# Performance work log

Measured on AMD Instinct MI355X. Metric: run time of the kernel, lower is better.

Reference implementation:

```python
import jax, jax.numpy as jnp
import numpy as np


def _dsepconv(inp, vert, horiz, offx, offy, mask):
    # inp: [B,C,H,W]; vert/horiz: [B,F,H,W]; offx/offy/mask: [B,F*F,H,W]
    B, C, H, W = inp.shape
    F = vert.shape[1]
    FF = F * F
    dt = inp.dtype
    k = jnp.arange(FF)
    ki = (k // F).astype(dt)   # vertical tap index i
    kj = (k % F).astype(dt)    # horizontal tap index j
    half = jnp.asarray((F - 1) / 2.0, dt)
    ys = jnp.arange(H, dtype=dt)
    xs = jnp.arange(W, dtype=dt)
    # per-pixel deformable sample positions, [B,FF,H,W]
    py = offy + ys[None, None, :, None] + (ki - half)[None, :, None, None]
    px = offx + xs[None, None, None, :] + (kj - half)[None, :, None, None]
    py = jnp.clip(py, 0.0, H - 1)
    px = jnp.clip(px, 0.0, W - 1)
    y0f = jnp.floor(py)
    x0f = jnp.floor(px)
    wy = py - y0f   # bilinear fractional weights
    wx = px - x0f
    y0 = y0f.astype(jnp.int32)
    x0 = x0f.astype(jnp.int32)
    y1 = jnp.minimum(y0 + 1, H - 1)
    x1 = jnp.minimum(x0 + 1, W - 1)

    inp_flat = inp.reshape(B, C, H * W)

    def gather(yi, xi):
        # flat spatial gather per batch element -> [B,C,FF,H,W]
        idx = (yi * W + xi).reshape(B, FF * H * W)
        g = jax.vmap(lambda im, ix: im[:, ix])(inp_flat, idx)
        return g.reshape(B, C, FF, H, W)

    g00 = gather(y0, x0)
    g01 = gather(y0, x1)
    g10 = gather(y1, x0)
    g11 = gather(y1, x1)
    wy_ = wy[:, None]  # [B,1,FF,H,W]
    wx_ = wx[:, None]
    samp = (g00 * (1 - wy_) * (1 - wx_)
            + g01 * (1 - wy_) * wx_
            + g10 * wy_ * (1 - wx_)
            + g11 * wy_ * wx_)  # [B,C,FF,H,W]
    # separable mask-weighted tap weights: vert[i]*horiz[j]*mask[k]
    wtap = vert[:, k // F] * horiz[:, k % F] * mask  # [B,FF,H,W]
    return jnp.einsum('bkhw,bckhw->bchw', wtap, samp)


def setup_inputs() -> dict:
    key = jax.random.key(0)
    ks = jax.random.split(key, 6)
    B, C, H, W, F = 4, 3, 384, 384, 5
    return {
        'tensorInput': jax.random.normal(ks[0], (B, C, H, W), jnp.float32),
        'tensorVertical': jax.random.uniform(ks[1], (B, F, H, W), jnp.float32),
        'tensorHorizontal': jax.random.uniform(ks[2], (B, F, H, W), jnp.float32),
        'tensorOffsetX': jax.random.normal(ks[3], (B, F * F, H, W), jnp.float32),
        'tensorOffsetY': jax.random.normal(ks[4], (B, F * F, H, W), jnp.float32),
        'tensorMask': jax.random.uniform(ks[5], (B, F * F, H, W), jnp.float32),
    }


def reference(tensorInput, tensorVertical, tensorHorizontal, tensorOffsetX, tensorOffsetY, tensorMask):
    return _dsepconv(tensorInput, tensorVertical, tensorHorizontal,
                     tensorOffsetX, tensorOffsetY, tensorMask)
```

## Files before the change

### kernel.cpp

```cpp
#include <hip/hip_runtime.h>
#include <hip/hip_fp16.h>

#define BB 4
#define CC 3
#define HH 384
#define WW 384
#define FF 5
#define KK 25
#define HW (HH*WW)
#define WP 192
#define TOT (BB*HH*WP)

#define TX 64
#define TY 8

typedef float fx2 __attribute__((ext_vector_type(2)));

__device__ __forceinline__ fx2 nt_load2(const float* p) {
    return __builtin_nontemporal_load((const fx2*)p);
}

__device__ __forceinline__ uint2 pack_px(float c0, float c1, float c2) {
    __half2 h01 = __floats2half2_rn(c0, c1);
    uint2 r;
    r.x = *(const unsigned int*)&h01;
    r.y = (unsigned int)__half_as_ushort(__float2half_rn(c2));
    return r;
}

__global__ __launch_bounds__(256) void pack_kernel(
    const float* __restrict__ inp, uint4* __restrict__ tab)
{
    int t = blockIdx.x * blockDim.x + threadIdx.x;
    if (t >= TOT) return;
    int j = t % WP;
    int y = (t / WP) % HH;
    int b = t / (WP * HH);
    int p0 = 2 * j, p1 = 2 * j + 1, p2 = min(2 * j + 2, WW - 1);
    const float* b0 = inp + (((size_t)b * CC + 0) * HH + y) * WW;
    const float* b1 = inp + (((size_t)b * CC + 1) * HH + y) * WW;
    const float* b2 = inp + (((size_t)b * CC + 2) * HH + y) * WW;
    uint2 q0 = pack_px(b0[p0], b1[p0], b2[p0]);
    uint2 q1 = pack_px(b0[p1], b1[p1], b2[p1]);
    uint2 q2 = pack_px(b0[p2], b1[p2], b2[p2]);
    tab[t]       = make_uint4(q0.x, q0.y, q1.x, q1.y);
    tab[TOT + t] = make_uint4(q1.x, q1.y, q2.x, q2.y);
}

__device__ __forceinline__ void unpack_pair(uint4 r,
    float& lo0, float& lo1, float& lo2, float& hi0, float& hi1, float& hi2)
{
    float2 lo01 = __half22float2(*(const __half2*)&r.x);
    float2 hi01 = __half22float2(*(const __half2*)&r.z);
    lo0 = lo01.x; lo1 = lo01.y;
    hi0 = hi01.x; hi1 = hi01.y;
    lo2 = __half2float(*(const __half*)&r.y);
    hi2 = __half2float(*(const __half*)&r.w);
}

__global__ __launch_bounds__(256) void dsepconv_kernel(
    const uint4* __restrict__ tab,
    const float* __restrict__ vert,
    const float* __restrict__ horiz,
    const float* __restrict__ offx,
    const float* __restrict__ offy,
    const float* __restrict__ mask,
    float* __restrict__ out)
{
    int tx = threadIdx.x & 31;
    int ty = threadIdx.x >> 5;
    int xb = blockIdx.x * TX + tx * 2;
    int y  = blockIdx.y * TY + ty;
    int b  = blockIdx.z;
    int planeoff = y * WW + xb;

    fx2 v2[FF], h2[FF];
#pragma unroll
    for (int f = 0; f < FF; ++f) {
        v2[f] = nt_load2(vert  + (b * FF + f) * HW + planeoff);
        h2[f] = nt_load2(horiz + (b * FF + f) * HW + planeoff);
    }

    const uint4* tb = tab + (size_t)b * (HH * WP);

    float acc[2][3] = {{0.f,0.f,0.f},{0.f,0.f,0.f}};
    const float fy = (float)y;

    for (int ki = 0; ki < FF; ++ki) {
        float dy = fy + (float)(ki - 2);
        const float* ox_p = offx + (size_t)(b * KK + ki * FF) * HW + planeoff;
        const float* oy_p = offy + (size_t)(b * KK + ki * FF) * HW + planeoff;
        const float* m_p  = mask + (size_t)(b * KK + ki * FF) * HW + planeoff;
#pragma unroll
        for (int kj = 0; kj < FF; ++kj) {
            fx2 ox2 = nt_load2(ox_p + kj * HW);
            fx2 oy2 = nt_load2(oy_p + kj * HW);
            fx2 m2  = nt_load2(m_p  + kj * HW);
#pragma unroll
            for (int p = 0; p < 2; ++p) {
                float wt = v2[ki][p] * h2[kj][p] * m2[p];
                float py = oy2[p] + dy;
                float px = ox2[p] + (float)(xb + p + kj - 2);
                py = fminf(fmaxf(py, 0.f), (float)(HH - 1));
                px = fminf(fmaxf(px, 0.f), (float)(WW - 1));
                float y0f = floorf(py);
                float x0f = floorf(px);
                float wy = py - y0f;
                float wx = px - x0f;
                int y0 = (int)y0f;
                int x0 = (int)x0f;
                int y1 = min(y0 + 1, HH - 1);

                int j    = x0 >> 1;
                const uint4* tbs = tb + ((x0 & 1) ? TOT : 0);
                uint4 r0 = tbs[y0 * WP + j];
                uint4 r1 = tbs[y1 * WP + j];

                float a00,a01,a02,b00,b01,b02;
                float a10,a11,a12,b10,b11,b12;
                unpack_pair(r0, a00,a01,a02, b00,b01,b02);
                unpack_pair(r1, a10,a11,a12, b10,b11,b12);

                float w00 = (1.f - wy) * (1.f - wx);
                float w01 = (1.f - wy) * wx;
                float w10 = wy * (1.f - wx);
                float w11 = wy * wx;

                acc[p][0] += wt * (a00*w00 + b00*w01 + a10*w10 + b10*w11);
                acc[p][1] += wt * (a01*w00 + b01*w01 + a11*w10 + b11*w11);
                acc[p][2] += wt * (a02*w00 + b02*w01 + a12*w10 + b12*w11);
            }
        }
    }

#pragma unroll
    for (int c = 0; c < CC; ++c) {
        fx2 o; o.x = acc[0][c]; o.y = acc[1][c];
        *(fx2*)(out + ((size_t)b * CC + c) * HW + planeoff) = o;
    }
}

extern "C" void kernel_launch(void* const* d_in, const int* in_sizes, int n_in,
                              void* d_out, int out_size, void* d_ws, size_t ws_size,
                              hipStream_t stream) {
    const float* inp   = (const float*)d_in[0];
    const float* vert  = (const float*)d_in[1];
    const float* horiz = (const float*)d_in[2];
    const float* offx  = (const float*)d_in[3];
    const float* offy  = (const float*)d_in[4];
    const float* mask  = (const float*)d_in[5];
    float* out = (float*)d_out;
    uint4* tab = (uint4*)d_ws;

    {
        pack_kernel<<<(TOT + 255) / 256, 256, 0, stream>>>(inp, tab);
    }
    {
        dim3 grid(WW / TX, HH / TY, BB);
        dsepconv_kernel<<<grid, 256, 0, stream>>>(
            tab, vert, horiz, offx, offy, mask, out);
    }
}
```

Baseline: 219.3 us.

## Stage packed halo tile in LDS for bilinear gathers with global fallback

Each block now copies a halo region of the packed fp16 pixel table (28 rows by 45 column pairs, both parity variants) into shared memory. Bilinear taps are read from LDS, with a fallback to fp32 global loads for samples outside the halo. The pack kernel now uses vector loads, and the bilinear blend becomes nested lerps. This is meant to replace scattered global/L2 gathers with LDS reads, at the cost of about 41KB of LDS per block (lower occupancy), a sync, and divergent fallback paths.

```diff
diff --git a/kernel.cpp b/kernel.cpp
--- a/kernel.cpp
+++ b/kernel.cpp
@@ -13,6 +13,14 @@
 
 #define TX 64
 #define TY 8
+#define MX 10
+#define MY 9
+#define RH 28
+#define NJP 45
+#define RS 1488
+#define BOFF 720
+#define SENT (RH*2*NJP)
+#define LDSB (RH*RS)
 
 typedef float fx2 __attribute__((ext_vector_type(2)));
 
@@ -36,30 +44,25 @@
     int j = t % WP;
     int y = (t / WP) % HH;
     int b = t / (WP * HH);
-    int p0 = 2 * j, p1 = 2 * j + 1, p2 = min(2 * j + 2, WW - 1);
+    int p0 = 2 * j;
+    int p2 = min(2 * j + 2, WW - 1);
     const float* b0 = inp + (((size_t)b * CC + 0) * HH + y) * WW;
     const float* b1 = inp + (((size_t)b * CC + 1) * HH + y) * WW;
     const float* b2 = inp + (((size_t)b * CC + 2) * HH + y) * WW;
-    uint2 q0 = pack_px(b0[p0], b1[p0], b2[p0]);
-    uint2 q1 = pack_px(b0[p1], b1[p1], b2[p1]);
-    uint2 q2 = pack_px(b0[p2], b1[p2], b2[p2]);
+    fx2 a0 = *(const fx2*)(b0 + p0);
+    fx2 a1 = *(const fx2*)(b1 + p0);
+    fx2 a2 = *(const fx2*)(b2 + p0);
+    float c0 = b0[p2], c1 = b1[p2], c2 = b2[p2];
+    uint2 q0 = pack_px(a0.x, a1.x, a2.x);
+    uint2 q1 = pack_px(a0.y, a1.y, a2.y);
+    uint2 q2 = pack_px(c0, c1, c2);
     tab[t]       = make_uint4(q0.x, q0.y, q1.x, q1.y);
     tab[TOT + t] = make_uint4(q1.x, q1.y, q2.x, q2.y);
 }
 
-__device__ __forceinline__ void unpack_pair(uint4 r,
-    float& lo0, float& lo1, float& lo2, float& hi0, float& hi1, float& hi2)
-{
-    float2 lo01 = __half22float2(*(const __half2*)&r.x);
-    float2 hi01 = __half22float2(*(const __half2*)&r.z);
-    lo0 = lo01.x; lo1 = lo01.y;
-    hi0 = hi01.x; hi1 = hi01.y;
-    lo2 = __half2float(*(const __half*)&r.y);
-    hi2 = __half2float(*(const __half*)&r.w);
-}
-
 __global__ __launch_bounds__(256) void dsepconv_kernel(
     const uint4* __restrict__ tab,
+    const float* __restrict__ inp,
     const float* __restrict__ vert,
     const float* __restrict__ horiz,
     const float* __restrict__ offx,
@@ -67,12 +70,32 @@
     const float* __restrict__ mask,
     float* __restrict__ out)
 {
+    __shared__ __align__(16) unsigned char lds_raw[LDSB];
+
     int tx = threadIdx.x & 31;
     int ty = threadIdx.x >> 5;
-    int xb = blockIdx.x * TX + tx * 2;
-    int y  = blockIdx.y * TY + ty;
+    int X  = blockIdx.x * TX;
+    int Y  = blockIdx.y * TY;
+    int xb = X + tx * 2;
+    int y  = Y + ty;
     int b  = blockIdx.z;
+    int ylo = Y - MY, xlo = X - MX;
+    int jp_base = xlo >> 1;
     int planeoff = y * WW + xb;
+
+    const uint4* tA = tab + (size_t)b * (HH * WP);
+    const uint4* tB = tA + TOT;
+    for (int p = threadIdx.x; p < SENT; p += 256) {
+        int r = p / (2 * NJP);
+        int c = p - r * (2 * NJP);
+        int gy = min(max(ylo + r, 0), HH - 1);
+        int idx = (c < NJP) ? c : c - NJP;
+        int jg  = min(max(jp_base + idx, 0), WP - 1);
+        const uint4* src = (c < NJP) ? tA : tB;
+        uint4 q = src[gy * WP + jg];
+        *(uint4*)(lds_raw + r * RS + c * 16) = q;
+    }
+    __syncthreads();
 
     fx2 v2[FF], h2[FF];
 #pragma unroll
@@ -81,7 +104,9 @@
         h2[f] = nt_load2(horiz + (b * FF + f) * HW + planeoff);
     }
 
-    const uint4* tb = tab + (size_t)b * (HH * WP);
+    const float* c0p = inp + ((size_t)b * CC + 0) * HW;
+    const float* c1p = inp + ((size_t)b * CC + 1) * HW;
+    const float* c2p = inp + ((size_t)b * CC + 2) * HW;
 
     float acc[2][3] = {{0.f,0.f,0.f},{0.f,0.f,0.f}};
     const float fy = (float)y;
@@ -109,26 +134,54 @@
                 float wx = px - x0f;
                 int y0 = (int)y0f;
                 int x0 = (int)x0f;
-                int y1 = min(y0 + 1, HH - 1);
-
-                int j    = x0 >> 1;
-                const uint4* tbs = tb + ((x0 & 1) ? TOT : 0);
-                uint4 r0 = tbs[y0 * WP + j];
-                uint4 r1 = tbs[y1 * WP + j];
-
-                float a00,a01,a02,b00,b01,b02;
-                float a10,a11,a12,b10,b11,b12;
-                unpack_pair(r0, a00,a01,a02, b00,b01,b02);
-                unpack_pair(r1, a10,a11,a12, b10,b11,b12);
-
-                float w00 = (1.f - wy) * (1.f - wx);
-                float w01 = (1.f - wy) * wx;
-                float w10 = wy * (1.f - wx);
-                float w11 = wy * wx;
-
-                acc[p][0] += wt * (a00*w00 + b00*w01 + a10*w10 + b10*w11);
-                acc[p][1] += wt * (a01*w00 + b01*w01 + a11*w10 + b11*w11);
-                acc[p][2] += wt * (a02*w00 + b02*w01 + a12*w10 + b12*w11);
+
+                int y0r = y0 - ylo;
+                int jpl = (x0 >> 1) - jp_base;
+                bool ok = ((unsigned)y0r <= (unsigned)(RH - 2)) &
+                          ((unsigned)jpl <= (unsigned)(NJP - 1));
+                int yc = min(max(y0r, 0), RH - 2);
+                int jc = min(max(jpl, 0), NJP - 1);
+                int off = yc * RS + jc * 16 + ((x0 & 1) ? BOFF : 0);
+
+                uint4 r0 = *(const uint4*)(lds_raw + off);
+                uint4 r1 = *(const uint4*)(lds_raw + off + RS);
+
+                float2 f0 = __half22float2(*(const __half2*)&r0.x);
+                float2 g0 = __half22float2(*(const __half2*)&r0.z);
+                float2 f1 = __half22float2(*(const __half2*)&r1.x);
+                float2 g1 = __half22float2(*(const __half2*)&r1.z);
+                float a0c0 = f0.x, a0c1 = f0.y;
+                float b0c0 = g0.x, b0c1 = g0.y;
+                float a1c0 = f1.x, a1c1 = f1.y;
+                float b1c0 = g1.x, b1c1 = g1.y;
+                float a0c2 = __half2float(*(const __half*)&r0.y);
+                float b0c2 = __half2float(*(const __half*)&r0.w);
+                float a1c2 = __half2float(*(const __half*)&r1.y);
+                float b1c2 = __half2float(*(const __half*)&r1.w);
+
+                if (__builtin_expect(!__all((int)ok), 0)) {
+                    if (!ok) {
+                        int x1  = min(x0 + 1, WW - 1);
+                        int y1g = min(y0 + 1, HH - 1);
+                        int o00 = y0 * WW + x0,  o01 = y0 * WW + x1;
+                        int o10 = y1g * WW + x0, o11 = y1g * WW + x1;
+                        a0c0 = c0p[o00]; a0c1 = c1p[o00]; a0c2 = c2p[o00];
+                        b0c0 = c0p[o01]; b0c1 = c1p[o01]; b0c2 = c2p[o01];
+                        a1c0 = c0p[o10]; a1c1 = c1p[o10]; a1c2 = c2p[o10];
+                        b1c0 = c0p[o11]; b1c1 = c1p[o11]; b1c2 = c2p[o11];
+                    }
+                }
+
+                float t0, t1;
+                t0 = a0c0 + wx * (b0c0 - a0c0);
+                t1 = a1c0 + wx * (b1c0 - a1c0);
+                acc[p][0] += wt * (t0 + wy * (t1 - t0));
+                t0 = a0c1 + wx * (b0c1 - a0c1);
+                t1 = a1c1 + wx * (b1c1 - a1c1);
+                acc[p][1] += wt * (t0 + wy * (t1 - t0));
+                t0 = a0c2 + wx * (b0c2 - a0c2);
+                t1 = a1c2 + wx * (b1c2 - a1c2);
+                acc[p][2] += wt * (t0 + wy * (t1 - t0));
             }
         }
     }
@@ -158,6 +211,6 @@
     {
         dim3 grid(WW / TX, HH / TY, BB);
         dsepconv_kernel<<<grid, 256, 0, stream>>>(
-            tab, vert, horiz, offx, offy, mask, out);
-    }
-}
+            tab, inp, vert, horiz, offx, offy, mask, out);
+    }
+}
```

Result: slower. 259.4 us (+18.3%).
